# Optimization experiments

Measured on AMD Instinct MI355X. Metric: run time of the kernel, lower is better.

Reference implementation:

```python
import jax, jax.numpy as jnp
import numpy as np

D_MODEL = 1024
N_HEADS = 16
WINDOW = 64
GLOBAL_RATIO = 0.1
HEAD_DIM = D_MODEL // N_HEADS
NEG_INF = -1e9  # matches torch float32 branch of _get_neg_inf
B, L = 1, 2048


def setup_inputs() -> dict:
    key = jax.random.key(0)
    ks = jax.random.split(key, 6)
    x = jax.random.normal(ks[0], (B, L, D_MODEL), jnp.float32)
    s = 1.0 / np.sqrt(D_MODEL)  # nn.Linear default init bound

    def lin(k):
        k1, k2 = jax.random.split(k)
        W = jax.random.uniform(k1, (D_MODEL, D_MODEL), jnp.float32, -s, s)
        b = jax.random.uniform(k2, (D_MODEL,), jnp.float32, -s, s)
        return W, b

    Wq, bq = lin(ks[1])
    Wk, bk = lin(ks[2])
    Wv, bv = lin(ks[3])
    Wo, bo = lin(ks[4])
    n_global = max(1, int(L * GLOBAL_RATIO))  # 204
    global_indices = jnp.sort(jax.random.randint(ks[5], (n_global,), 0, L))
    return dict(x=x, Wq=Wq, bq=bq, Wk=Wk, bk=bk, Wv=Wv, bv=bv, Wo=Wo, bo=bo,
                global_indices=global_indices)


def reference(x, Wq, bq, Wk, bk, Wv, bv, Wo, bo, global_indices):
    Bb, Ll, Dm = x.shape
    H, Dh = N_HEADS, HEAD_DIM
    scale = 1.0 / jnp.sqrt(jnp.float32(Dh))
    # projections (torch Linear: y = x @ W.T + b)
    Q = (x @ Wq.T + bq).reshape(Bb, Ll, H, Dh)
    K = (x @ Wk.T + bk).reshape(Bb, Ll, H, Dh)
    V = (x @ Wv.T + bv).reshape(Bb, Ll, H, Dh)

    # --- local sliding-window attention (vectorized version of the per-i loop) ---
    half = WINDOW // 2
    W = WINDOW + 1  # positions i-half .. i+half inclusive
    pos = jnp.arange(Ll)[:, None] + jnp.arange(-half, half + 1)[None, :]  # [L,W]
    valid = (pos >= 0) & (pos < Ll)          # edge truncation == masking to -inf
    posc = jnp.clip(pos, 0, Ll - 1)
    Kw = K[:, posc]                           # [B,L,W,H,Dh]
    Vw = V[:, posc]
    s_loc = jnp.einsum('blhd,blwhd->bhlw', Q, Kw) * scale
    s_loc = jnp.where(valid[None, None], s_loc, NEG_INF)
    a_loc = jax.nn.softmax(s_loc, axis=-1)
    local = jnp.einsum('bhlw,blwhd->blhd', a_loc, Vw)

    # --- global random-token attention ---
    Kg = K[:, global_indices]                 # [B,G,H,Dh]
    Vg = V[:, global_indices]
    s_g = jnp.einsum('blhd,bghd->bhlg', Q, Kg) * scale
    a_g = jax.nn.softmax(s_g, axis=-1)
    glob = jnp.einsum('bhlg,bghd->blhd', a_g, Vg)

    out = 0.7 * local + 0.3 * glob
    return out.reshape(Bb, Ll, Dm) @ Wo.T + bo
```

## Files before the change

kernel.cpp:

```cpp
#include <hip/hip_runtime.h>
#include <hip/hip_bf16.h>
#include <stdint.h>

#define L_SEQ 2048
#define D_MODEL 1024
#define NH 16
#define DH 64
#define NEG_INF -1e9f

typedef short bf16x4 __attribute__((ext_vector_type(4)));
typedef short bf16x8 __attribute__((ext_vector_type(8)));
typedef float f32x4 __attribute__((ext_vector_type(4)));
typedef unsigned short ushort_t;
typedef const __attribute__((address_space(1))) void* gas_t;
typedef __attribute__((address_space(3))) void* las_t;

#define MFMA16(a, b, c) __builtin_amdgcn_mfma_f32_16x16x32_bf16((a), (b), (c), 0, 0, 0)

__device__ __forceinline__ ushort_t f2b(float f) {
  union { float f; unsigned u; } v; v.f = f;
  unsigned r = v.u + 0x7fffu + ((v.u >> 16) & 1u);
  return (ushort_t)(r >> 16);
}

__global__ __launch_bounds__(256) void cvt_kernel(
    const float* __restrict__ x, const float* __restrict__ wq,
    const float* __restrict__ wk, const float* __restrict__ wv,
    const float* __restrict__ wo, ushort_t* __restrict__ out) {
  long e = ((long)blockIdx.x * 256 + threadIdx.x) * 4;
  const float* src; long off;
  if (e < 2097152L)      { src = x;  off = e; }
  else if (e < 3145728L) { src = wq; off = e - 2097152L; }
  else if (e < 4194304L) { src = wk; off = e - 3145728L; }
  else if (e < 5242880L) { src = wv; off = e - 4194304L; }
  else                   { src = wo; off = e - 5242880L; }
  float4 v = *(const float4*)(src + off);
  ushort4 o;
  o.x = f2b(v.x); o.y = f2b(v.y); o.z = f2b(v.z); o.w = f2b(v.w);
  *(ushort4*)(out + e) = o;
}

__global__ __launch_bounds__(512, 4) void gemm_qkv(
    const ushort_t* __restrict__ A, const ushort_t* __restrict__ Wbase,
    const float* __restrict__ b0, const float* __restrict__ b1,
    const float* __restrict__ b2, ushort_t* __restrict__ outbase) {
  const int z = blockIdx.z;
  const ushort_t* W = Wbase + (long)z * (D_MODEL * D_MODEL);
  const float* bias = (z == 0) ? b0 : ((z == 1) ? b1 : b2);
  const float scale = (z == 0) ? 0.125f : 1.0f;

  __shared__ ushort_t As[4 * 128 * 32];
  __shared__ ushort_t Bs[4 * 128 * 32];
  const int tid = threadIdx.x;
  const int lane = tid & 63;
  const int wid = tid >> 6;
  const int wm = wid >> 2, wn = wid & 3;
  const int m0 = blockIdx.x * 128, n0 = blockIdx.y * 128;
  const int K = D_MODEL;
  const int l15 = lane & 15, lg8 = (lane >> 4) * 8;

  const int soff = tid * 16;
  const int srow = soff >> 6;
  const int scol = (soff & 63) >> 1;

  const ushort_t* Aptr = A + (long)(m0 + srow) * K + scol;
  const ushort_t* Wptr = W + (long)(n0 + srow) * K + scol;

  auto stage = [&](int buf, int step) {
    __builtin_amdgcn_global_load_lds(
        (gas_t)(const void*)(Aptr + step * 32),
        (las_t)(void*)((char*)As + buf * 8192 + soff), 16, 0, 0);
    __builtin_amdgcn_global_load_lds(
        (gas_t)(const void*)(Wptr + step * 32),
        (las_t)(void*)((char*)Bs + buf * 8192 + soff), 16, 0, 0);
  };

  f32x4 acc[4][2] = {};

  auto compute = [&](int buf) {
    const ushort_t* Ab = As + buf * (128 * 32);
    const ushort_t* Bb = Bs + buf * (128 * 32);
    bf16x8 af[4], bf[2];
#pragma unroll
    for (int t = 0; t < 4; ++t)
      af[t] = *(const bf16x8*)(Ab + (wm * 64 + t * 16 + l15) * 32 + lg8);
#pragma unroll
    for (int t = 0; t < 2; ++t)
      bf[t] = *(const bf16x8*)(Bb + (wn * 32 + t * 16 + l15) * 32 + lg8);
#pragma unroll
    for (int mt = 0; mt < 4; ++mt)
#pragma unroll
      for (int nt = 0; nt < 2; ++nt)
        acc[mt][nt] = MFMA16(af[mt], bf[nt], acc[mt][nt]);
  };

  const int NSTEP = K / 32;
  stage(0, 0);
  stage(1, 1);
  for (int s = 0; s < NSTEP - 2; ++s) {
    stage((s + 2) & 3, s + 2);
    asm volatile("s_waitcnt vmcnt(4)" ::: "memory");
    __builtin_amdgcn_s_barrier();
    __builtin_amdgcn_sched_barrier(0);
    compute(s & 3);
  }
  asm volatile("s_waitcnt vmcnt(2)" ::: "memory");
  __builtin_amdgcn_s_barrier();
  __builtin_amdgcn_sched_barrier(0);
  compute((NSTEP - 2) & 3);
  asm volatile("s_waitcnt vmcnt(0)" ::: "memory");
  __builtin_amdgcn_s_barrier();
  __builtin_amdgcn_sched_barrier(0);
  compute((NSTEP - 1) & 3);

  const int lg4 = (lane >> 4) * 4;
  ushort_t* o = outbase + (long)z * ((long)NH * L_SEQ * DH);
#pragma unroll
  for (int mt = 0; mt < 4; ++mt)
#pragma unroll
    for (int nt = 0; nt < 2; ++nt)
#pragma unroll
      for (int r = 0; r < 4; ++r) {
        int row = m0 + wm * 64 + mt * 16 + lg4 + r;
        int col = n0 + wn * 32 + nt * 16 + l15;
        float v = (acc[mt][nt][r] + bias[col]) * scale;
        o[((long)(col >> 6) * L_SEQ + row) * DH + (col & 63)] = f2b(v);
      }
}

__global__ __launch_bounds__(256, 3) void gemm_out(
    const ushort_t* __restrict__ A, const ushort_t* __restrict__ W,
    const float* __restrict__ bias, float* __restrict__ o) {
  __shared__ ushort_t As[4 * 128 * 32];
  __shared__ ushort_t Bs[4 * 64 * 32];
  const int tid = threadIdx.x;
  const int lane = tid & 63;
  const int wid = tid >> 6;
  const int wm = wid >> 1, wn = wid & 1;
  const int m0 = blockIdx.x * 128, n0 = blockIdx.y * 64;
  const int K = D_MODEL;
  const int l15 = lane & 15, lg8 = (lane >> 4) * 8;

  const int soff = tid * 16;
  const int srow = soff >> 6;
  const int scol = (soff & 63) >> 1;

  const ushort_t* Aptr0 = A + (long)(m0 + srow) * K + scol;
  const ushort_t* Aptr1 = A + (long)(m0 + 64 + srow) * K + scol;
  const ushort_t* Wptr  = W + (long)(n0 + srow) * K + scol;

  auto stage = [&](int buf, int step) {
    __builtin_amdgcn_global_load_lds(
        (gas_t)(const void*)(Aptr0 + step * 32),
        (las_t)(void*)((char*)As + buf * 8192 + soff), 16, 0, 0);
    __builtin_amdgcn_global_load_lds(
        (gas_t)(const void*)(Aptr1 + step * 32),
        (las_t)(void*)((char*)As + buf * 8192 + 4096 + soff), 16, 0, 0);
    __builtin_amdgcn_global_load_lds(
        (gas_t)(const void*)(Wptr + step * 32),
        (las_t)(void*)((char*)Bs + buf * 4096 + soff), 16, 0, 0);
  };

  f32x4 acc[4][2] = {};

  auto compute = [&](int buf) {
    const ushort_t* Ab = As + buf * (128 * 32);
    const ushort_t* Bb = Bs + buf * (64 * 32);
    bf16x8 af[4], bf[2];
#pragma unroll
    for (int t = 0; t < 4; ++t)
      af[t] = *(const bf16x8*)(Ab + (wm * 64 + t * 16 + l15) * 32 + lg8);
#pragma unroll
    for (int t = 0; t < 2; ++t)
      bf[t] = *(const bf16x8*)(Bb + (wn * 32 + t * 16 + l15) * 32 + lg8);
#pragma unroll
    for (int mt = 0; mt < 4; ++mt)
#pragma unroll
      for (int nt = 0; nt < 2; ++nt)
        acc[mt][nt] = MFMA16(af[mt], bf[nt], acc[mt][nt]);
  };

  const int NSTEP = K / 32;
  stage(0, 0);
  stage(1, 1);
  for (int s = 0; s < NSTEP - 2; ++s) {
    stage((s + 2) & 3, s + 2);
    asm volatile("s_waitcnt vmcnt(6)" ::: "memory");
    __builtin_amdgcn_s_barrier();
    __builtin_amdgcn_sched_barrier(0);
    compute(s & 3);
  }
  asm volatile("s_waitcnt vmcnt(3)" ::: "memory");
  __builtin_amdgcn_s_barrier();
  __builtin_amdgcn_sched_barrier(0);
  compute((NSTEP - 2) & 3);
  asm volatile("s_waitcnt vmcnt(0)" ::: "memory");
  __builtin_amdgcn_s_barrier();
  __builtin_amdgcn_sched_barrier(0);
  compute((NSTEP - 1) & 3);

  const int lg4 = (lane >> 4) * 4;
#pragma unroll
  for (int mt = 0; mt < 4; ++mt)
#pragma unroll
    for (int nt = 0; nt < 2; ++nt)
#pragma unroll
      for (int r = 0; r < 4; ++r) {
        int row = m0 + wm * 64 + mt * 16 + lg4 + r;
        int col = n0 + wn * 32 + nt * 16 + l15;
        o[(long)row * D_MODEL + col] = acc[mt][nt][r] + bias[col];
      }
}

#define STK 356
__global__ __launch_bounds__(256) void attn_kernel(
    const ushort_t* __restrict__ QKV, const int* __restrict__ gidx, int NG,
    ushort_t* __restrict__ attn_out) {
  __shared__ ushort_t smem[352 * 72];

  const int tid = threadIdx.x;
  const int lane = tid & 63;
  const int w = tid >> 6;
  const int h = blockIdx.y;
  const int q0 = blockIdx.x * 64;

  const long hoff = (long)h * L_SEQ * DH;
  const ushort_t* Qh = QKV + hoff;
  const ushort_t* Kh = QKV + (long)NH * L_SEQ * DH + hoff;
  const ushort_t* Vh = QKV + 2L * NH * L_SEQ * DH + hoff;

  const int rr = tid >> 3;
  const int c8 = (tid & 7) * 8;

  ushort_t* kb0 = smem;
  ushort_t* kb1 = smem + 128 * 72;
  ushort_t* kb2 = smem + 256 * 72;

#pragma unroll
  for (int it = 0; it < 4; ++it) {
    int r = rr + it * 32;
    int sr = q0 - 32 + r;
    sr = sr < 0 ? 0 : (sr > L_SEQ - 1 ? L_SEQ - 1 : sr);
    int4 v = *(const int4*)(Kh + (long)sr * DH + c8);
    *(int4*)(kb0 + r * 72 + c8) = v;
  }
#pragma unroll
  for (int it = 0; it < 4; ++it) {
    int r = rr + it * 32;
    int idx = r < NG ? r : NG - 1;
    int4 v = *(const int4*)(Kh + (long)gidx[idx] * DH + c8);
    *(int4*)(kb1 + r * 72 + c8) = v;
  }
#pragma unroll
  for (int it = 0; it < 3; ++it) {
    int r = rr + it * 32;
    int i = 128 + r;
    int idx = i < NG ? i : NG - 1;
    int4 v = *(const int4*)(Kh + (long)gidx[idx] * DH + c8);
    *(int4*)(kb2 + r * 72 + c8) = v;
  }
  __syncthreads();

  const int l15 = lane & 15, lg = lane >> 4;
  const int ql = q0 + w * 16 + l15;
  bf16x8 qf0 = *(const bf16x8*)(Qh + (long)ql * DH + lg * 8);
  bf16x8 qf1 = *(const bf16x8*)(Qh + (long)ql * DH + 32 + lg * 8);

  f32x4 sl[8], sg[14];
#pragma unroll
  for (int kt = 0; kt < 8; ++kt) {
    f32x4 c = {};
    bf16x8 k0 = *(const bf16x8*)(kb0 + (kt * 16 + l15) * 72 + lg * 8);
    bf16x8 k1 = *(const bf16x8*)(kb0 + (kt * 16 + l15) * 72 + 32 + lg * 8);
    c = MFMA16(k0, qf0, c);
    c = MFMA16(k1, qf1, c);
    sl[kt] = c;
  }
#pragma unroll
  for (int kt = 0; kt < 8; ++kt) {
    f32x4 c = {};
    bf16x8 k0 = *(const bf16x8*)(kb1 + (kt * 16 + l15) * 72 + lg * 8);
    bf16x8 k1 = *(const bf16x8*)(kb1 + (kt * 16 + l15) * 72 + 32 + lg * 8);
    c = MFMA16(k0, qf0, c);
    c = MFMA16(k1, qf1, c);
    sg[kt] = c;
  }
#pragma unroll
  for (int kt = 0; kt < 6; ++kt) {
    f32x4 c = {};
    bf16x8 k0 = *(const bf16x8*)(kb2 + (kt * 16 + l15) * 72 + lg * 8);
    bf16x8 k1 = *(const bf16x8*)(kb2 + (kt * 16 + l15) * 72 + 32 + lg * 8);
    c = MFMA16(k0, qf0, c);
    c = MFMA16(k1, qf1, c);
    sg[8 + kt] = c;
  }
  __syncthreads();

  int4 vst[11];
#pragma unroll
  for (int it = 0; it < 4; ++it) {
    int r = rr + it * 32;
    int sr = q0 - 32 + r;
    sr = sr < 0 ? 0 : (sr > L_SEQ - 1 ? L_SEQ - 1 : sr);
    vst[it] = *(const int4*)(Vh + (long)sr * DH + c8);
  }
#pragma unroll
  for (int it = 0; it < 4; ++it) {
    int r = rr + it * 32;
    int idx = r < NG ? r : NG - 1;
    vst[4 + it] = *(const int4*)(Vh + (long)gidx[idx] * DH + c8);
  }
#pragma unroll
  for (int it = 0; it < 3; ++it) {
    int i = 128 + rr + it * 32;
    int idx = i < NG ? i : NG - 1;
    vst[8 + it] = *(const int4*)(Vh + (long)gidx[idx] * DH + c8);
  }

  float mx = NEG_INF;
#pragma unroll
  for (int kt = 0; kt < 8; ++kt)
#pragma unroll
    for (int r4 = 0; r4 < 4; ++r4) {
      int key = q0 - 32 + kt * 16 + lg * 4 + r4;
      int d = key - ql;
      bool valid = (key >= 0) && (key < L_SEQ) && (d <= 32) && (d >= -32);
      float v = valid ? sl[kt][r4] : NEG_INF;
      sl[kt][r4] = v;
      mx = fmaxf(mx, v);
    }
  mx = fmaxf(mx, __shfl_xor(mx, 16, 64));
  mx = fmaxf(mx, __shfl_xor(mx, 32, 64));
  float den = 0.f;
#pragma unroll
  for (int kt = 0; kt < 8; ++kt)
#pragma unroll
    for (int r4 = 0; r4 < 4; ++r4) {
      float e = __expf(sl[kt][r4] - mx);
      sl[kt][r4] = e;
      den += e;
    }
  den += __shfl_xor(den, 16, 64);
  den += __shfl_xor(den, 32, 64);
  const float psl = 0.7f / den;

  float mg = NEG_INF;
#pragma unroll
  for (int t = 0; t < 14; ++t)
#pragma unroll
    for (int r4 = 0; r4 < 4; ++r4) {
      int i = t * 16 + lg * 4 + r4;
      float v = (i < NG) ? sg[t][r4] : NEG_INF;
      sg[t][r4] = v;
      mg = fmaxf(mg, v);
    }
  mg = fmaxf(mg, __shfl_xor(mg, 16, 64));
  mg = fmaxf(mg, __shfl_xor(mg, 32, 64));
  float deng = 0.f;
#pragma unroll
  for (int t = 0; t < 14; ++t)
#pragma unroll
    for (int r4 = 0; r4 < 4; ++r4) {
      float e = __expf(sg[t][r4] - mg);
      sg[t][r4] = e;
      deng += e;
    }
  deng += __shfl_xor(deng, 16, 64);
  deng += __shfl_xor(deng, 32, 64);
  const float psg = 0.3f / deng;

  bf16x8 pl[4], pg[7];
#pragma unroll
  for (int s = 0; s < 4; ++s)
#pragma unroll
    for (int j = 0; j < 4; ++j) {
      pl[s][j]     = (short)f2b(sl[2 * s][j] * psl);
      pl[s][j + 4] = (short)f2b(sl[2 * s + 1][j] * psl);
    }
#pragma unroll
  for (int s = 0; s < 7; ++s)
#pragma unroll
    for (int j = 0; j < 4; ++j) {
      pg[s][j]     = (short)f2b(sg[2 * s][j] * psg);
      pg[s][j + 4] = (short)f2b(sg[2 * s + 1][j] * psg);
    }

#pragma unroll
  for (int it = 0; it < 4; ++it) {
    int r = rr + it * 32;
    ushort_t tmp[8]; *(int4*)tmp = vst[it];
#pragma unroll
    for (int j = 0; j < 8; ++j) smem[(c8 + j) * STK + r] = tmp[j];
  }
#pragma unroll
  for (int it = 0; it < 4; ++it) {
    int r = 128 + rr + it * 32;
    ushort_t tmp[8]; *(int4*)tmp = vst[4 + it];
#pragma unroll
    for (int j = 0; j < 8; ++j) smem[(c8 + j) * STK + r] = tmp[j];
  }
#pragma unroll
  for (int it = 0; it < 3; ++it) {
    int r = 256 + rr + it * 32;
    ushort_t tmp[8]; *(int4*)tmp = vst[8 + it];
#pragma unroll
    for (int j = 0; j < 8; ++j) smem[(c8 + j) * STK + r] = tmp[j];
  }
  __syncthreads();

  f32x4 o4[4];
#pragma unroll
  for (int dt = 0; dt < 4; ++dt) {
    f32x4 c = {};
    const ushort_t* vrow = smem + (dt * 16 + l15) * STK + lg * 4;
#pragma unroll
    for (int s = 0; s < 11; ++s) {
      bf16x4 lo = *(const bf16x4*)(vrow + s * 32);
      bf16x4 hi = *(const bf16x4*)(vrow + s * 32 + 16);
      bf16x8 vf = __builtin_shufflevector(lo, hi, 0, 1, 2, 3, 4, 5, 6, 7);
      c = MFMA16(s < 4 ? pl[s] : pg[s - 4], vf, c);
    }
    o4[dt] = c;
  }

#pragma unroll
  for (int dt = 0; dt < 4; ++dt)
#pragma unroll
    for (int r4 = 0; r4 < 4; ++r4) {
      int row = q0 + w * 16 + lg * 4 + r4;
      int dc = dt * 16 + l15;
      attn_out[(long)row * D_MODEL + h * DH + dc] = f2b(o4[dt][r4]);
    }
}

extern "C" void kernel_launch(void* const* d_in, const int* in_sizes, int n_in,
                              void* d_out, int out_size, void* d_ws, size_t ws_size,
                              hipStream_t stream) {
  const float* x  = (const float*)d_in[0];
  const float* Wq = (const float*)d_in[1];
  const float* bq = (const float*)d_in[2];
  const float* Wk = (const float*)d_in[3];
  const float* bk = (const float*)d_in[4];
  const float* Wv = (const float*)d_in[5];
  const float* bv = (const float*)d_in[6];
  const float* Wo = (const float*)d_in[7];
  const float* bo = (const float*)d_in[8];
  const int* gidx = (const int*)d_in[9];
  const int NG = in_sizes[9];

  ushort_t* ws = (ushort_t*)d_ws;
  ushort_t* xb   = ws;
  ushort_t* wb   = ws + 2097152L;
  ushort_t* qkv  = ws + 6291456L;
  ushort_t* attn = ws + 12582912L;

  cvt_kernel<<<6144, 256, 0, stream>>>(x, Wq, Wk, Wv, Wo, ws);
  gemm_qkv<<<dim3(16, 8, 3), 512, 0, stream>>>(xb, wb, bq, bk, bv, qkv);
  attn_kernel<<<dim3(32, 16), 256, 0, stream>>>(qkv, gidx, NG, attn);
  gemm_out<<<dim3(16, 16), 256, 0, stream>>>(attn, wb + 3145728L, bo,
                                             (float*)d_out);
}
```

Before: 65.57 us.

## Split attention into separate local and global kernels with larger global tiles

```diff
diff --git a/kernel.cpp b/kernel.cpp
--- a/kernel.cpp
+++ b/kernel.cpp
@@ -21,6 +21,9 @@
   union { float f; unsigned u; } v; v.f = f;
   unsigned r = v.u + 0x7fffu + ((v.u >> 16) & 1u);
   return (ushort_t)(r >> 16);
+}
+__device__ __forceinline__ float b2f(ushort_t u) {
+  union { unsigned u; float f; } v; v.u = ((unsigned)u) << 16; return v.f;
 }
 
 __global__ __launch_bounds__(256) void cvt_kernel(
@@ -212,11 +215,10 @@
       }
 }
 
-#define STK 356
-__global__ __launch_bounds__(256) void attn_kernel(
-    const ushort_t* __restrict__ QKV, const int* __restrict__ gidx, int NG,
-    ushort_t* __restrict__ attn_out) {
-  __shared__ ushort_t smem[352 * 72];
+__global__ __launch_bounds__(256) void attn_local(
+    const ushort_t* __restrict__ QKV, ushort_t* __restrict__ attnL) {
+  __shared__ ushort_t kb[128 * 72];
+  __shared__ ushort_t vt[64 * 132];
 
   const int tid = threadIdx.x;
   const int lane = tid & 63;
@@ -232,32 +234,13 @@
   const int rr = tid >> 3;
   const int c8 = (tid & 7) * 8;
 
-  ushort_t* kb0 = smem;
-  ushort_t* kb1 = smem + 128 * 72;
-  ushort_t* kb2 = smem + 256 * 72;
-
 #pragma unroll
   for (int it = 0; it < 4; ++it) {
     int r = rr + it * 32;
     int sr = q0 - 32 + r;
     sr = sr < 0 ? 0 : (sr > L_SEQ - 1 ? L_SEQ - 1 : sr);
     int4 v = *(const int4*)(Kh + (long)sr * DH + c8);
-    *(int4*)(kb0 + r * 72 + c8) = v;
-  }
-#pragma unroll
-  for (int it = 0; it < 4; ++it) {
-    int r = rr + it * 32;
-    int idx = r < NG ? r : NG - 1;
-    int4 v = *(const int4*)(Kh + (long)gidx[idx] * DH + c8);
-    *(int4*)(kb1 + r * 72 + c8) = v;
-  }
-#pragma unroll
-  for (int it = 0; it < 3; ++it) {
-    int r = rr + it * 32;
-    int i = 128 + r;
-    int idx = i < NG ? i : NG - 1;
-    int4 v = *(const int4*)(Kh + (long)gidx[idx] * DH + c8);
-    *(int4*)(kb2 + r * 72 + c8) = v;
+    *(int4*)(kb + r * 72 + c8) = v;
   }
   __syncthreads();
 
@@ -266,55 +249,24 @@
   bf16x8 qf0 = *(const bf16x8*)(Qh + (long)ql * DH + lg * 8);
   bf16x8 qf1 = *(const bf16x8*)(Qh + (long)ql * DH + 32 + lg * 8);
 
-  f32x4 sl[8], sg[14];
+  f32x4 sl[8];
 #pragma unroll
   for (int kt = 0; kt < 8; ++kt) {
     f32x4 c = {};
-    bf16x8 k0 = *(const bf16x8*)(kb0 + (kt * 16 + l15) * 72 + lg * 8);
-    bf16x8 k1 = *(const bf16x8*)(kb0 + (kt * 16 + l15) * 72 + 32 + lg * 8);
+    bf16x8 k0 = *(const bf16x8*)(kb + (kt * 16 + l15) * 72 + lg * 8);
+    bf16x8 k1 = *(const bf16x8*)(kb + (kt * 16 + l15) * 72 + 32 + lg * 8);
     c = MFMA16(k0, qf0, c);
     c = MFMA16(k1, qf1, c);
     sl[kt] = c;
   }
-#pragma unroll
-  for (int kt = 0; kt < 8; ++kt) {
-    f32x4 c = {};
-    bf16x8 k0 = *(const bf16x8*)(kb1 + (kt * 16 + l15) * 72 + lg * 8);
-    bf16x8 k1 = *(const bf16x8*)(kb1 + (kt * 16 + l15) * 72 + 32 + lg * 8);
-    c = MFMA16(k0, qf0, c);
-    c = MFMA16(k1, qf1, c);
-    sg[kt] = c;
-  }
-#pragma unroll
-  for (int kt = 0; kt < 6; ++kt) {
-    f32x4 c = {};
-    bf16x8 k0 = *(const bf16x8*)(kb2 + (kt * 16 + l15) * 72 + lg * 8);
-    bf16x8 k1 = *(const bf16x8*)(kb2 + (kt * 16 + l15) * 72 + 32 + lg * 8);
-    c = MFMA16(k0, qf0, c);
-    c = MFMA16(k1, qf1, c);
-    sg[8 + kt] = c;
-  }
-  __syncthreads();
-
-  int4 vst[11];
+
+  int4 vst[4];
 #pragma unroll
   for (int it = 0; it < 4; ++it) {
     int r = rr + it * 32;
     int sr = q0 - 32 + r;
     sr = sr < 0 ? 0 : (sr > L_SEQ - 1 ? L_SEQ - 1 : sr);
     vst[it] = *(const int4*)(Vh + (long)sr * DH + c8);
-  }
-#pragma unroll
-  for (int it = 0; it < 4; ++it) {
-    int r = rr + it * 32;
-    int idx = r < NG ? r : NG - 1;
-    vst[4 + it] = *(const int4*)(Vh + (long)gidx[idx] * DH + c8);
-  }
-#pragma unroll
-  for (int it = 0; it < 3; ++it) {
-    int i = 128 + rr + it * 32;
-    int idx = i < NG ? i : NG - 1;
-    vst[8 + it] = *(const int4*)(Vh + (long)gidx[idx] * DH + c8);
   }
 
   float mx = NEG_INF;
@@ -344,9 +296,102 @@
   den += __shfl_xor(den, 32, 64);
   const float psl = 0.7f / den;
 
+  bf16x8 pl[4];
+#pragma unroll
+  for (int s = 0; s < 4; ++s)
+#pragma unroll
+    for (int j = 0; j < 4; ++j) {
+      pl[s][j]     = (short)f2b(sl[2 * s][j] * psl);
+      pl[s][j + 4] = (short)f2b(sl[2 * s + 1][j] * psl);
+    }
+
+#pragma unroll
+  for (int it = 0; it < 4; ++it) {
+    int r = rr + it * 32;
+    ushort_t tmp[8]; *(int4*)tmp = vst[it];
+#pragma unroll
+    for (int j = 0; j < 8; ++j) vt[(c8 + j) * 132 + r] = tmp[j];
+  }
+  __syncthreads();
+
+#pragma unroll
+  for (int dt = 0; dt < 4; ++dt) {
+    f32x4 c = {};
+    const ushort_t* vrow = vt + (dt * 16 + l15) * 132 + lg * 4;
+#pragma unroll
+    for (int s = 0; s < 4; ++s) {
+      bf16x4 lo = *(const bf16x4*)(vrow + s * 32);
+      bf16x4 hi = *(const bf16x4*)(vrow + s * 32 + 16);
+      bf16x8 vf = __builtin_shufflevector(lo, hi, 0, 1, 2, 3, 4, 5, 6, 7);
+      c = MFMA16(pl[s], vf, c);
+    }
+#pragma unroll
+    for (int r4 = 0; r4 < 4; ++r4) {
+      int row = q0 + w * 16 + lg * 4 + r4;
+      attnL[(long)row * D_MODEL + h * DH + dt * 16 + l15] = f2b(c[r4]);
+    }
+  }
+}
+
+#define VTW 228
+__global__ __launch_bounds__(512) void attn_glob(
+    const ushort_t* __restrict__ QKV, const int* __restrict__ gidx, int NG,
+    const ushort_t* __restrict__ attnL, ushort_t* __restrict__ attn_out) {
+  __shared__ ushort_t kg[208 * 72];
+  __shared__ ushort_t vtg[64 * VTW];
+
+  const int tid = threadIdx.x;
+  const int lane = tid & 63;
+  const int w = tid >> 6;
+  const int h = blockIdx.y;
+  const int q0 = blockIdx.x * 128;
+
+  const long hoff = (long)h * L_SEQ * DH;
+  const ushort_t* Qh = QKV + hoff;
+  const ushort_t* Kh = QKV + (long)NH * L_SEQ * DH + hoff;
+  const ushort_t* Vh = QKV + 2L * NH * L_SEQ * DH + hoff;
+
+#pragma unroll
+  for (int it = 0; it < 4; ++it) {
+    int c = tid + it * 512;
+    if (c < 1664) {
+      int r = c >> 3, cc = (c & 7) * 8;
+      int idx = r < NG ? r : NG - 1;
+      int4 v = *(const int4*)(Kh + (long)gidx[idx] * DH + cc);
+      *(int4*)(kg + r * 72 + cc) = v;
+    }
+  }
+  __syncthreads();
+
+  const int l15 = lane & 15, lg = lane >> 4;
+  const int ql = q0 + w * 16 + l15;
+  bf16x8 qf0 = *(const bf16x8*)(Qh + (long)ql * DH + lg * 8);
+  bf16x8 qf1 = *(const bf16x8*)(Qh + (long)ql * DH + 32 + lg * 8);
+
+  f32x4 sg[13];
+#pragma unroll
+  for (int kt = 0; kt < 13; ++kt) {
+    f32x4 c = {};
+    bf16x8 k0 = *(const bf16x8*)(kg + (kt * 16 + l15) * 72 + lg * 8);
+    bf16x8 k1 = *(const bf16x8*)(kg + (kt * 16 + l15) * 72 + 32 + lg * 8);
+    c = MFMA16(k0, qf0, c);
+    c = MFMA16(k1, qf1, c);
+    sg[kt] = c;
+  }
+
+  int4 vst[4];
+#pragma unroll
+  for (int it = 0; it < 4; ++it) {
+    int c = tid + it * 512;
+    int cl = c < 1664 ? c : 1663;
+    int r = cl >> 3, cc = (cl & 7) * 8;
+    int idx = r < NG ? r : NG - 1;
+    vst[it] = *(const int4*)(Vh + (long)gidx[idx] * DH + cc);
+  }
+
   float mg = NEG_INF;
 #pragma unroll
-  for (int t = 0; t < 14; ++t)
+  for (int t = 0; t < 13; ++t)
 #pragma unroll
     for (int r4 = 0; r4 < 4; ++r4) {
       int i = t * 16 + lg * 4 + r4;
@@ -358,7 +403,7 @@
   mg = fmaxf(mg, __shfl_xor(mg, 32, 64));
   float deng = 0.f;
 #pragma unroll
-  for (int t = 0; t < 14; ++t)
+  for (int t = 0; t < 13; ++t)
 #pragma unroll
     for (int r4 = 0; r4 < 4; ++r4) {
       float e = __expf(sg[t][r4] - mg);
@@ -369,68 +414,52 @@
   deng += __shfl_xor(deng, 32, 64);
   const float psg = 0.3f / deng;
 
-  bf16x8 pl[4], pg[7];
-#pragma unroll
-  for (int s = 0; s < 4; ++s)
-#pragma unroll
-    for (int j = 0; j < 4; ++j) {
-      pl[s][j]     = (short)f2b(sl[2 * s][j] * psl);
-      pl[s][j + 4] = (short)f2b(sl[2 * s + 1][j] * psl);
-    }
-#pragma unroll
-  for (int s = 0; s < 7; ++s)
+  bf16x8 pg[7];
+#pragma unroll
+  for (int s = 0; s < 6; ++s)
 #pragma unroll
     for (int j = 0; j < 4; ++j) {
       pg[s][j]     = (short)f2b(sg[2 * s][j] * psg);
       pg[s][j + 4] = (short)f2b(sg[2 * s + 1][j] * psg);
     }
-
-#pragma unroll
-  for (int it = 0; it < 4; ++it) {
-    int r = rr + it * 32;
-    ushort_t tmp[8]; *(int4*)tmp = vst[it];
-#pragma unroll
-    for (int j = 0; j < 8; ++j) smem[(c8 + j) * STK + r] = tmp[j];
-  }
-#pragma unroll
-  for (int it = 0; it < 4; ++it) {
-    int r = 128 + rr + it * 32;
-    ushort_t tmp[8]; *(int4*)tmp = vst[4 + it];
-#pragma unroll
-    for (int j = 0; j < 8; ++j) smem[(c8 + j) * STK + r] = tmp[j];
-  }
-#pragma unroll
-  for (int it = 0; it < 3; ++it) {
-    int r = 256 + rr + it * 32;
-    ushort_t tmp[8]; *(int4*)tmp = vst[8 + it];
-#pragma unroll
-    for (int j = 0; j < 8; ++j) smem[(c8 + j) * STK + r] = tmp[j];
-  }
+#pragma unroll
+  for (int j = 0; j < 4; ++j) {
+    pg[6][j]     = (short)f2b(sg[12][j] * psg);
+    pg[6][j + 4] = 0;
+  }
+
+#pragma unroll
+  for (int it = 0; it < 4; ++it) {
+    int c = tid + it * 512;
+    if (c < 1664) {
+      int r = c >> 3, cc = (c & 7) * 8;
+      ushort_t tmp[8]; *(int4*)tmp = vst[it];
+#pragma unroll
+      for (int j = 0; j < 8; ++j) vtg[(cc + j) * VTW + r] = tmp[j];
+    }
+  }
+  for (int i = tid; i < 64 * 20; i += 512)
+    vtg[(i / 20) * VTW + 208 + (i % 20)] = 0;
   __syncthreads();
 
-  f32x4 o4[4];
 #pragma unroll
   for (int dt = 0; dt < 4; ++dt) {
     f32x4 c = {};
-    const ushort_t* vrow = smem + (dt * 16 + l15) * STK + lg * 4;
-#pragma unroll
-    for (int s = 0; s < 11; ++s) {
+    const ushort_t* vrow = vtg + (dt * 16 + l15) * VTW + lg * 4;
+#pragma unroll
+    for (int s = 0; s < 7; ++s) {
       bf16x4 lo = *(const bf16x4*)(vrow + s * 32);
       bf16x4 hi = *(const bf16x4*)(vrow + s * 32 + 16);
       bf16x8 vf = __builtin_shufflevector(lo, hi, 0, 1, 2, 3, 4, 5, 6, 7);
-      c = MFMA16(s < 4 ? pl[s] : pg[s - 4], vf, c);
-    }
-    o4[dt] = c;
-  }
-
-#pragma unroll
-  for (int dt = 0; dt < 4; ++dt)
+      c = MFMA16(pg[s], vf, c);
+    }
 #pragma unroll
     for (int r4 = 0; r4 < 4; ++r4) {
       int row = q0 + w * 16 + lg * 4 + r4;
-      int dc = dt * 16 + l15;
-      attn_out[(long)row * D_MODEL + h * DH + dc] = f2b(o4[dt][r4]);
-    }
+      long off = (long)row * D_MODEL + h * DH + dt * 16 + l15;
+      attn_out[off] = f2b(b2f(attnL[off]) + c[r4]);
+    }
+  }
 }
 
 extern "C" void kernel_launch(void* const* d_in, const int* in_sizes, int n_in,
@@ -449,14 +478,16 @@
   const int NG = in_sizes[9];
 
   ushort_t* ws = (ushort_t*)d_ws;
-  ushort_t* xb   = ws;
-  ushort_t* wb   = ws + 2097152L;
-  ushort_t* qkv  = ws + 6291456L;
-  ushort_t* attn = ws + 12582912L;
+  ushort_t* xb    = ws;
+  ushort_t* wb    = ws + 2097152L;
+  ushort_t* qkv   = ws + 6291456L;
+  ushort_t* attn  = ws + 12582912L;
+  ushort_t* attnL = ws + 14680064L;
 
   cvt_kernel<<<6144, 256, 0, stream>>>(x, Wq, Wk, Wv, Wo, ws);
   gemm_qkv<<<dim3(16, 8, 3), 512, 0, stream>>>(xb, wb, bq, bk, bv, qkv);
-  attn_kernel<<<dim3(32, 16), 256, 0, stream>>>(qkv, gidx, NG, attn);
+  attn_local<<<dim3(32, 16), 256, 0, stream>>>(qkv, attnL);
+  attn_glob<<<dim3(16, 16), 512, 0, stream>>>(qkv, gidx, NG, attnL, attn);
   gemm_out<<<dim3(16, 16), 256, 0, stream>>>(attn, wb + 3145728L, bo,
                                              (float*)d_out);
 }
```

Measured after the change: 63.60 us. -3.0%, faster.
